# Optimization experiments

Hardware: AMD Instinct MI355X
Metric: run time of the kernel (lower is better)

Reference implementation:

```python
import jax, jax.numpy as jnp
import numpy as np

# Module constants derived from default grid_config
D = 59          # depth bins: (60-1)/1
C_OUT = 64
X, Y, Z = 128, 128, 7
STRIDE = 16
GRID_LB = np.array([-51.2, -51.2, -2.5], dtype=np.float32)
GRID_IV = np.array([0.8, 0.8, 1.0], dtype=np.float32)
D0, DSTEP = 1.0, 1.0

B, N, C_IN, H, W = 4, 6, 256, 16, 44


def _voxel_coords():
    xs, ys, zs = np.meshgrid(np.arange(X), np.arange(Y), np.arange(Z), indexing='ij')
    coords = np.stack([xs, ys, zs], axis=-1).reshape(-1, 3).astype(np.float32)
    coords = coords * GRID_IV + GRID_LB  # [V, 3] ego-frame voxel centers
    return coords


def _camera_rig(rng):
    """Realistic 6-camera rig: yawed cameras looking outward, z_cam = forward."""
    c2e = np.zeros((B, N, 4, 4), dtype=np.float32)
    K = np.zeros((B, N, 3, 3), dtype=np.float32)
    for b in range(B):
        for n in range(N):
            a = 2.0 * np.pi * n / N + 0.02 * rng.standard_normal()
            f = np.array([np.cos(a), np.sin(a), 0.0])           # camera forward (z_cam)
            x_cam = np.array([-np.sin(a), np.cos(a), 0.0])      # camera right
            y_cam = np.array([0.0, 0.0, -1.0])                   # camera down
            R = np.stack([x_cam, y_cam, f], axis=1)              # columns = cam axes in ego
            t = 1.0 * f + np.array([0.0, 0.0, 1.5])
            c2e[b, n, :3, :3] = R
            c2e[b, n, :3, 3] = t
            c2e[b, n, 3, 3] = 1.0
            fl = 400.0 + 5.0 * rng.standard_normal()
            K[b, n] = np.array([[fl, 0.0, 352.0], [0.0, fl, 128.0], [0.0, 0.0, 1.0]])
    return c2e, K


def setup_inputs() -> dict:
    key = jax.random.key(0)
    k1, k2, k3 = jax.random.split(key, 3)
    img_feats = jax.random.normal(k1, (B, N, C_IN, H, W), dtype=jnp.float32)
    c2e, K = _camera_rig(np.random.default_rng(0))
    # depth_net: 1x1 conv in_channels -> D + C_OUT
    w_depth = jax.random.normal(k2, (D + C_OUT, C_IN), dtype=jnp.float32) * (1.0 / np.sqrt(C_IN))
    b_depth = jax.random.normal(k3, (D + C_OUT,), dtype=jnp.float32) * 0.01
    return {
        'img_feats': img_feats,
        'cam2ego': jnp.asarray(c2e),
        'cam_intrinsics': jnp.asarray(K),
        'w_depth': w_depth,
        'b_depth': b_depth,
    }


def reference(img_feats, cam2ego, cam_intrinsics, w_depth, b_depth):
    Bc, Nc, C, Hc, Wc = img_feats.shape
    # 1x1 conv == per-pixel linear
    x = jnp.einsum('bnchw,oc->bnhwo', img_feats, w_depth) + b_depth  # [B,N,H,W,D+C_OUT]
    depth = jax.nn.softmax(x[..., :D], axis=-1)                      # [B,N,H,W,D]
    feat = x[..., D:]                                                # [B,N,H,W,C_OUT]

    vox = jnp.asarray(_voxel_coords())                               # [V,3]
    V = vox.shape[0]
    vox_h = jnp.concatenate([vox, jnp.ones((V, 1), vox.dtype)], axis=1)  # [V,4]

    e2c = jnp.linalg.inv(cam2ego)                                    # [B,N,4,4]
    cam = jnp.einsum('bnij,vj->bnvi', e2c, vox_h)[..., :3]           # [B,N,V,3]
    z = cam[..., 2]
    z_safe = jnp.maximum(z, 0.1)
    norm = cam[..., :2] / z_safe[..., None]
    homo = jnp.concatenate([norm, jnp.ones_like(z[..., None])], axis=-1)  # [B,N,V,3]
    img = jnp.einsum('bnij,bnvj->bnvi', cam_intrinsics, homo)[..., :2]
    fc = img / STRIDE                                                # feature-plane coords

    depth_bin = ((z - D0) / DSTEP).astype(jnp.int32)                 # trunc toward 0, matches .long()
    valid = (
        (fc[..., 0] >= 0) & (fc[..., 0] < Wc)
        & (fc[..., 1] >= 0) & (fc[..., 1] < Hc)
        & (z > 0.5)
        & (depth_bin >= 0) & (depth_bin < D)
    )

    u = jnp.clip(fc[..., 0].astype(jnp.int32), 0, Wc - 1)            # [B,N,V]
    v = jnp.clip(fc[..., 1].astype(jnp.int32), 0, Hc - 1)
    d = jnp.clip(depth_bin, 0, D - 1)
    hw = v * Wc + u

    feat_flat = feat.reshape(Bc, Nc, Hc * Wc, C_OUT)
    sampled_feat = jnp.take_along_axis(feat_flat, hw[..., None], axis=2)   # [B,N,V,C_OUT]
    depth_flat = depth.reshape(Bc, Nc, Hc * Wc * D)
    sampled_depth = jnp.take_along_axis(depth_flat, hw * D + d, axis=2)    # [B,N,V]

    wgt = sampled_depth * valid.astype(sampled_depth.dtype)
    # scatter_add at flat_idx == voxel index (identity) -> masked sum over cameras
    bev = jnp.einsum('bnv,bnvc->bvc', wgt, sampled_feat)             # [B,V,C_OUT]
    bev = bev.reshape(Bc, X, Y, Z, C_OUT).sum(axis=3)                # collapse Z
    bev = bev.transpose(0, 3, 2, 1)                                  # [B,C_OUT,Y,X]
    return bev, depth
```

## Files before the change

kernel.cpp:

```cpp
#include <hip/hip_runtime.h>
#include <math.h>

#define D_BINS 59
#define CO     64
#define CI     256
#define NB     4
#define NC     6
#define H_IMG  16
#define W_IMG  44
#define HW     704
#define NPIX   (NB*NC*HW)
#define XD     128
#define YD     128
#define ZD     7
#define NOUT   123
#define PXB    66
#define THR    384
#define XW     66

typedef float v2f __attribute__((ext_vector_type(2)));

__device__ void inv_rigid(const float* __restrict__ M, float* __restrict__ o) {
    double a = M[0], b = M[1], c = M[2], t0 = M[3];
    double d = M[4], e = M[5], f = M[6], t1 = M[7];
    double g = M[8], h = M[9], ii = M[10], t2 = M[11];
    double A00 = e*ii - f*h, A01 = c*h - b*ii, A02 = b*f - c*e;
    double A10 = f*g - d*ii, A11 = a*ii - c*g, A12 = c*d - a*f;
    double A20 = d*h - e*g,  A21 = b*g - a*h,  A22 = a*e - b*d;
    double det = a*A00 + b*A10 + c*A20;
    double inv = 1.0 / det;
    double r00 = A00*inv, r01 = A01*inv, r02 = A02*inv;
    double r10 = A10*inv, r11 = A11*inv, r12 = A12*inv;
    double r20 = A20*inv, r21 = A21*inv, r22 = A22*inv;
    o[0] = (float)r00; o[1] = (float)r01; o[2]  = (float)r02;
    o[3] = (float)(-(r00*t0 + r01*t1 + r02*t2));
    o[4] = (float)r10; o[5] = (float)r11; o[6]  = (float)r12;
    o[7] = (float)(-(r10*t0 + r11*t1 + r12*t2));
    o[8] = (float)r20; o[9] = (float)r21; o[10] = (float)r22;
    o[11] = (float)(-(r20*t0 + r21*t1 + r22*t2));
}

__global__ __launch_bounds__(256) void k_pre(
    const float* __restrict__ wd, const float* __restrict__ c2e,
    float* __restrict__ wt2, float* __restrict__ e2c) {
    const int o = blockIdx.x;
    const int k = threadIdx.x;
    float v = (o < NOUT) ? wd[(size_t)o * CI + k] : 0.f;
    wt2[(size_t)(k >> 1) * 256 + o * 2 + (k & 1)] = v;
    if (blockIdx.x == 0 && k < NB * NC)
        inv_rigid(c2e + k * 16, e2c + k * 12);
}

__global__ __launch_bounds__(THR) void k_head(
    const float* __restrict__ img, const float* __restrict__ wt2,
    const float* __restrict__ bd, float* __restrict__ depth_out,
    float* __restrict__ feat_ws) {
    __shared__ float A[64 / 2 * 132];
    __shared__ float X[PXB * XW];
    __shared__ float S[PXB];

    const int tid  = threadIdx.x;
    const int wv   = tid >> 6;
    const int ln   = tid & 63;
    const int p0   = blockIdx.x * PXB;
    const int half = blockIdx.y;
    const int ob   = half << 6;
    const bool is_main = (wv < 4);
    const int o0   = __builtin_amdgcn_readfirstlane(ob + ((is_main ? wv : 0) << 4));
    const int epx  = 64 + (wv - 4);

    int a_off[11];
    int g_off[11];
#pragma unroll
    for (int it = 0; it < 11; ++it) {
        int idx = tid + it * THR;
        int kl = idx / PXB, px = idx - kl * PXB;
        int p = p0 + px;
        int bn = p / HW, hw = p - bn * HW;
        a_off[it] = (kl >> 1) * 132 + px * 2 + (kl & 1);
        g_off[it] = (bn * CI + kl) * HW + hw;
    }

    v2f acc[16];
#pragma unroll
    for (int j = 0; j < 16; ++j) acc[j] = (v2f)(0.f);
    v2f acc2 = (v2f)(0.f);

    for (int kc = 0; kc < 4; ++kc) {
#pragma unroll
        for (int it = 0; it < 11; ++it)
            A[a_off[it]] = img[g_off[it] + kc * 64 * HW];
        __syncthreads();

        if (is_main) {
#pragma unroll 4
            for (int k2 = 0; k2 < 32; ++k2) {
                v2f a = *(const v2f*)(A + k2 * 132 + ln * 2);
                const v2f* w =
                    (const v2f*)(wt2 + (size_t)(kc * 32 + k2) * 256) + o0;
#pragma unroll
                for (int j = 0; j < 16; ++j)
                    acc[j] = __builtin_elementwise_fma(a, w[j], acc[j]);
            }
        } else {
#pragma unroll 4
            for (int k2 = 0; k2 < 32; ++k2) {
                v2f a = *(const v2f*)(A + k2 * 132 + epx * 2);
                const float* w = wt2 + (size_t)(kc * 32 + k2) * 256;
                v2f w0 = {w[(ob + ln) * 2], w[(ob + ln) * 2 + 1]};
                acc2 = __builtin_elementwise_fma(a, w0, acc2);
            }
        }
        __syncthreads();
    }

    if (is_main) {
#pragma unroll
        for (int j = 0; j < 16; ++j) {
            int o = o0 + j;
            if (o < NOUT)
                X[ln * XW + (o - ob)] = (acc[j].x + acc[j].y) + bd[o];
        }
    } else {
        int o = ob + ln;
        if (o < NOUT)
            X[epx * XW + ln] = (acc2.x + acc2.y) + bd[o];
    }
    __syncthreads();

    if (half == 0) {
        if (tid < PXB * 5) {
            int p = tid / 5, c = tid - p * 5;
            feat_ws[(size_t)(p0 + p) * CO + c] = X[p * XW + 59 + c];
        }
        if (tid < PXB) {
            float* row = X + tid * XW;
            float m = row[0];
            for (int o = 1; o < D_BINS; ++o) m = fmaxf(m, row[o]);
            float s = 0.f;
            for (int o = 0; o < D_BINS; ++o) {
                float e = __expf(row[o] - m);
                row[o] = e;
                s += e;
            }
            S[tid] = 1.f / s;
        }
        __syncthreads();
        for (int g = tid; g < PXB * D_BINS; g += THR) {
            int p = g / D_BINS;
            int o = g - p * D_BINS;
            depth_out[(size_t)p0 * D_BINS + g] = X[p * XW + o] * S[p];
        }
    } else {
        for (int g = tid; g < PXB * D_BINS; g += THR) {
            int p = g / D_BINS;
            int col = g - p * D_BINS;
            feat_ws[(size_t)(p0 + p) * CO + 5 + col] = X[p * XW + col];
        }
    }
}

__global__ __launch_bounds__(256) void k_splat(
    const float* __restrict__ e2c, const float* __restrict__ Kmat,
    const float* __restrict__ depth_g, const float* __restrict__ feat_ws,
    float* __restrict__ bev) {
    __shared__ int   hw_s[ZD][64];
    __shared__ float wgt_s[ZD][64];

    const int tx = threadIdx.x;
    const int cq = threadIdx.y;
    const int x = blockIdx.x * 64 + tx;
    const int y = blockIdx.y;
    const int b = blockIdx.z;
    const float wx = (float)x * 0.8f + (-51.2f);
    const float wy = (float)y * 0.8f + (-51.2f);

    float acc[16];
#pragma unroll
    for (int m = 0; m < 16; ++m) acc[m] = 0.f;

    for (int n = 0; n < NC; ++n) {
        const int bn = b * NC + n;
        const float* E = e2c + bn * 12;
        const float* Km = Kmat + bn * 9;
        const float k00 = Km[0], k01 = Km[1], k02 = Km[2];
        const float k10 = Km[3], k11 = Km[4], k12 = Km[5];
        const float e02 = E[2], e12 = E[6], e22 = E[10];
        const float bx0 = E[0] * wx + E[1] * wy + E[3];
        const float bx1 = E[4] * wx + E[5] * wy + E[7];
        const float bx2 = E[8] * wx + E[9] * wy + E[11];

#pragma unroll
        for (int zz = 0; zz < 2; ++zz) {
            const int z = cq + zz * 4;
            if (z < ZD) {
                const float wz = -2.5f + (float)z;
                const float cx = bx0 + e02 * wz;
                const float cy = bx1 + e12 * wz;
                const float cz = bx2 + e22 * wz;
                const float zs = fmaxf(cz, 0.1f);
                const float rz = 1.0f / zs;
                const float xn = cx * rz;
                const float yn = cy * rz;
                const float fu = (k00 * xn + k01 * yn + k02) * 0.0625f;
                const float fv = (k10 * xn + k11 * yn + k12) * 0.0625f;
                const int bin = (int)(cz - 1.0f);
                const bool valid = (fu >= 0.f) & (fu < (float)W_IMG) &
                                   (fv >= 0.f) & (fv < (float)H_IMG) &
                                   (cz > 0.5f) & (bin >= 0) & (bin < D_BINS);
                int hw = -1;
                float wgt = 0.f;
                if (valid) {
                    int u = (int)fu;
                    int v = (int)fv;
                    hw = v * W_IMG + u;
                    wgt = depth_g[((size_t)bn * HW + hw) * D_BINS + bin];
                }
                hw_s[z][tx] = hw;
                wgt_s[z][tx] = wgt;
            }
        }
        __syncthreads();

#pragma unroll
        for (int z = 0; z < ZD; ++z) {
            const int hw = hw_s[z][tx];
            if (hw >= 0) {
                const float wgt = wgt_s[z][tx];
                const float4* fp =
                    (const float4*)(feat_ws + ((size_t)bn * HW + hw) * CO + cq * 16);
                float4 f0 = fp[0], f1 = fp[1], f2 = fp[2], f3 = fp[3];
                acc[0]  = fmaf(wgt, f0.x, acc[0]);
                acc[1]  = fmaf(wgt, f0.y, acc[1]);
                acc[2]  = fmaf(wgt, f0.z, acc[2]);
                acc[3]  = fmaf(wgt, f0.w, acc[3]);
                acc[4]  = fmaf(wgt, f1.x, acc[4]);
                acc[5]  = fmaf(wgt, f1.y, acc[5]);
                acc[6]  = fmaf(wgt, f1.z, acc[6]);
                acc[7]  = fmaf(wgt, f1.w, acc[7]);
                acc[8]  = fmaf(wgt, f2.x, acc[8]);
                acc[9]  = fmaf(wgt, f2.y, acc[9]);
                acc[10] = fmaf(wgt, f2.z, acc[10]);
                acc[11] = fmaf(wgt, f2.w, acc[11]);
                acc[12] = fmaf(wgt, f3.x, acc[12]);
                acc[13] = fmaf(wgt, f3.y, acc[13]);
                acc[14] = fmaf(wgt, f3.z, acc[14]);
                acc[15] = fmaf(wgt, f3.w, acc[15]);
            }
        }
        __syncthreads();
    }
    float* ob = bev + (((size_t)b * CO + cq * 16) * YD + y) * XD + x;
#pragma unroll
    for (int m = 0; m < 16; ++m) ob[(size_t)m * YD * XD] = acc[m];
}

extern "C" void kernel_launch(void* const* d_in, const int* in_sizes, int n_in,
                              void* d_out, int out_size, void* d_ws, size_t ws_size,
                              hipStream_t stream) {
    const float* img  = (const float*)d_in[0];
    const float* c2e  = (const float*)d_in[1];
    const float* Kmat = (const float*)d_in[2];
    const float* wd   = (const float*)d_in[3];
    const float* bd   = (const float*)d_in[4];
    float* bev = (float*)d_out;
    float* depth_out = bev + (size_t)NB * CO * YD * XD;
    float* feat_ws = (float*)d_ws;
    float* wt2 = feat_ws + (size_t)NPIX * CO;
    float* e2c = wt2 + 128 * 256;

    k_pre<<<128, 256, 0, stream>>>(wd, c2e, wt2, e2c);
    k_head<<<dim3(256, 2), THR, 0, stream>>>(img, wt2, bd, depth_out, feat_ws);
    k_splat<<<dim3(2, YD, NB), dim3(64, 4, 1), 0, stream>>>(e2c, Kmat, depth_out,
                                                            feat_ws, bev);
}
```

Measured before the change: 122.5 us.

## Split K across two wave groups and load full input tile once

```diff
diff --git a/kernel.cpp b/kernel.cpp
--- a/kernel.cpp
+++ b/kernel.cpp
@@ -15,7 +15,7 @@
 #define ZD     7
 #define NOUT   123
 #define PXB    66
-#define THR    384
+#define THR    768
 #define XW     66
 
 typedef float v2f __attribute__((ext_vector_type(2)));
@@ -55,9 +55,8 @@
     const float* __restrict__ img, const float* __restrict__ wt2,
     const float* __restrict__ bd, float* __restrict__ depth_out,
     float* __restrict__ feat_ws) {
-    __shared__ float A[64 / 2 * 132];
-    __shared__ float X[PXB * XW];
-    __shared__ float S[PXB];
+    __shared__ float smem[128 * 132 + PXB];
+    float* S = smem + 128 * 132;
 
     const int tid  = threadIdx.x;
     const int wv   = tid >> 6;
@@ -65,66 +64,82 @@
     const int p0   = blockIdx.x * PXB;
     const int half = blockIdx.y;
     const int ob   = half << 6;
-    const bool is_main = (wv < 4);
-    const int o0   = __builtin_amdgcn_readfirstlane(ob + ((is_main ? wv : 0) << 4));
-    const int epx  = 64 + (wv - 4);
-
-    int a_off[11];
-    int g_off[11];
-#pragma unroll
-    for (int it = 0; it < 11; ++it) {
-        int idx = tid + it * THR;
+    const bool is_main = (wv < 8);
+    const int j    = wv & 3;
+    const int kh   = is_main ? (wv >> 2) : ((wv - 8) >> 1);
+    const int o0   = __builtin_amdgcn_readfirstlane(ob + (j << 4));
+    const int k2b  = __builtin_amdgcn_readfirstlane(kh << 6);
+    const int epx  = __builtin_amdgcn_readfirstlane(64 + ((wv - 8) & 1));
+
+    for (int idx = tid; idx < 256 * PXB; idx += THR) {
         int kl = idx / PXB, px = idx - kl * PXB;
         int p = p0 + px;
         int bn = p / HW, hw = p - bn * HW;
-        a_off[it] = (kl >> 1) * 132 + px * 2 + (kl & 1);
-        g_off[it] = (bn * CI + kl) * HW + hw;
-    }
+        smem[(kl >> 1) * 132 + px * 2 + (kl & 1)] =
+            img[((size_t)bn * CI + kl) * HW + hw];
+    }
+    __syncthreads();
 
     v2f acc[16];
 #pragma unroll
-    for (int j = 0; j < 16; ++j) acc[j] = (v2f)(0.f);
+    for (int q = 0; q < 16; ++q) acc[q] = (v2f)(0.f);
     v2f acc2 = (v2f)(0.f);
 
-    for (int kc = 0; kc < 4; ++kc) {
-#pragma unroll
-        for (int it = 0; it < 11; ++it)
-            A[a_off[it]] = img[g_off[it] + kc * 64 * HW];
-        __syncthreads();
-
+    if (is_main) {
+#pragma unroll 4
+        for (int k2i = 0; k2i < 64; ++k2i) {
+            int k2 = k2b + k2i;
+            v2f a = *(const v2f*)(smem + k2 * 132 + ln * 2);
+            const v2f* w = (const v2f*)(wt2 + (size_t)k2 * 256) + o0;
+#pragma unroll
+            for (int q = 0; q < 16; ++q)
+                acc[q] = __builtin_elementwise_fma(a, w[q], acc[q]);
+        }
+    } else {
+#pragma unroll 4
+        for (int k2i = 0; k2i < 64; ++k2i) {
+            int k2 = k2b + k2i;
+            v2f a = *(const v2f*)(smem + k2 * 132 + epx * 2);
+            const float* w = wt2 + (size_t)k2 * 256;
+            v2f w0 = {w[(ob + ln) * 2], w[(ob + ln) * 2 + 1]};
+            acc2 = __builtin_elementwise_fma(a, w0, acc2);
+        }
+    }
+    __syncthreads();
+
+    float* X = smem;
+    if (kh == 0) {
         if (is_main) {
-#pragma unroll 4
-            for (int k2 = 0; k2 < 32; ++k2) {
-                v2f a = *(const v2f*)(A + k2 * 132 + ln * 2);
-                const v2f* w =
-                    (const v2f*)(wt2 + (size_t)(kc * 32 + k2) * 256) + o0;
-#pragma unroll
-                for (int j = 0; j < 16; ++j)
-                    acc[j] = __builtin_elementwise_fma(a, w[j], acc[j]);
+#pragma unroll
+            for (int q = 0; q < 16; ++q) {
+                int o = o0 + q;
+                if (o < NOUT)
+                    X[ln * XW + (o - ob)] = acc[q].x + acc[q].y;
             }
         } else {
-#pragma unroll 4
-            for (int k2 = 0; k2 < 32; ++k2) {
-                v2f a = *(const v2f*)(A + k2 * 132 + epx * 2);
-                const float* w = wt2 + (size_t)(kc * 32 + k2) * 256;
-                v2f w0 = {w[(ob + ln) * 2], w[(ob + ln) * 2 + 1]};
-                acc2 = __builtin_elementwise_fma(a, w0, acc2);
-            }
-        }
-        __syncthreads();
-    }
-
-    if (is_main) {
-#pragma unroll
-        for (int j = 0; j < 16; ++j) {
-            int o = o0 + j;
+            int o = ob + ln;
             if (o < NOUT)
-                X[ln * XW + (o - ob)] = (acc[j].x + acc[j].y) + bd[o];
-        }
-    } else {
-        int o = ob + ln;
-        if (o < NOUT)
-            X[epx * XW + ln] = (acc2.x + acc2.y) + bd[o];
+                X[epx * XW + ln] = acc2.x + acc2.y;
+        }
+    }
+    __syncthreads();
+    if (kh == 1) {
+        if (is_main) {
+#pragma unroll
+            for (int q = 0; q < 16; ++q) {
+                int o = o0 + q;
+                if (o < NOUT) {
+                    int col = o - ob;
+                    X[ln * XW + col] =
+                        (X[ln * XW + col] + (acc[q].x + acc[q].y)) + bd[o];
+                }
+            }
+        } else {
+            int o = ob + ln;
+            if (o < NOUT)
+                X[epx * XW + ln] =
+                    (X[epx * XW + ln] + (acc2.x + acc2.y)) + bd[o];
+        }
     }
     __syncthreads();
 
```

Result: slower. 131.4 us (+7.2%).

## Double pixels per head block to reuse weight loads across two pixel sets

Applied to the files above, without the earlier changes.

```diff
diff --git a/kernel.cpp b/kernel.cpp
--- a/kernel.cpp
+++ b/kernel.cpp
@@ -14,7 +14,7 @@
 #define YD     128
 #define ZD     7
 #define NOUT   123
-#define PXB    66
+#define PXB    132
 #define THR    384
 #define XW     66
 
@@ -55,82 +55,89 @@
     const float* __restrict__ img, const float* __restrict__ wt2,
     const float* __restrict__ bd, float* __restrict__ depth_out,
     float* __restrict__ feat_ws) {
-    __shared__ float A[64 / 2 * 132];
-    __shared__ float X[PXB * XW];
-    __shared__ float S[PXB];
+    __shared__ float smem[PXB * XW + PXB];
+    float* S = smem + PXB * XW;
 
     const int tid  = threadIdx.x;
     const int wv   = tid >> 6;
     const int ln   = tid & 63;
     const int p0   = blockIdx.x * PXB;
-    const int half = blockIdx.y;
-    const int ob   = half << 6;
+    const int ob   = (int)blockIdx.y << 6;
     const bool is_main = (wv < 4);
     const int o0   = __builtin_amdgcn_readfirstlane(ob + ((is_main ? wv : 0) << 4));
-    const int epx  = 64 + (wv - 4);
-
-    int a_off[11];
-    int g_off[11];
-#pragma unroll
-    for (int it = 0; it < 11; ++it) {
-        int idx = tid + it * THR;
-        int kl = idx / PXB, px = idx - kl * PXB;
-        int p = p0 + px;
-        int bn = p / HW, hw = p - bn * HW;
-        a_off[it] = (kl >> 1) * 132 + px * 2 + (kl & 1);
-        g_off[it] = (bn * CI + kl) * HW + hw;
-    }
-
-    v2f acc[16];
-#pragma unroll
-    for (int j = 0; j < 16; ++j) acc[j] = (v2f)(0.f);
-    v2f acc2 = (v2f)(0.f);
-
+    const int e0   = 128 + (wv - 4);
+    const int e1   = 130 + (wv - 4);
+
+    v2f accA[16], accB[16];
+#pragma unroll
+    for (int j = 0; j < 16; ++j) { accA[j] = (v2f)(0.f); accB[j] = (v2f)(0.f); }
+    v2f acc2a = (v2f)(0.f), acc2b = (v2f)(0.f);
+
+    float* A = smem;
     for (int kc = 0; kc < 4; ++kc) {
 #pragma unroll
-        for (int it = 0; it < 11; ++it)
-            A[a_off[it]] = img[g_off[it] + kc * 64 * HW];
+        for (int it = 0; it < 22; ++it) {
+            int idx = tid + it * THR;
+            int kl = idx / PXB, px = idx - kl * PXB;
+            int p = p0 + px;
+            int bn = p / HW, hw = p - bn * HW;
+            A[(kl >> 1) * 264 + px * 2 + (kl & 1)] =
+                img[((size_t)bn * CI + kc * 64 + kl) * HW + hw];
+        }
         __syncthreads();
 
         if (is_main) {
 #pragma unroll 4
             for (int k2 = 0; k2 < 32; ++k2) {
-                v2f a = *(const v2f*)(A + k2 * 132 + ln * 2);
+                v2f aA = *(const v2f*)(A + k2 * 264 + ln * 2);
+                v2f aB = *(const v2f*)(A + k2 * 264 + (ln + 64) * 2);
                 const v2f* w =
                     (const v2f*)(wt2 + (size_t)(kc * 32 + k2) * 256) + o0;
 #pragma unroll
-                for (int j = 0; j < 16; ++j)
-                    acc[j] = __builtin_elementwise_fma(a, w[j], acc[j]);
+                for (int j = 0; j < 16; ++j) {
+                    v2f wj = w[j];
+                    accA[j] = __builtin_elementwise_fma(aA, wj, accA[j]);
+                    accB[j] = __builtin_elementwise_fma(aB, wj, accB[j]);
+                }
             }
         } else {
 #pragma unroll 4
             for (int k2 = 0; k2 < 32; ++k2) {
-                v2f a = *(const v2f*)(A + k2 * 132 + epx * 2);
+                v2f a0 = *(const v2f*)(A + k2 * 264 + e0 * 2);
+                v2f a1 = *(const v2f*)(A + k2 * 264 + e1 * 2);
                 const float* w = wt2 + (size_t)(kc * 32 + k2) * 256;
                 v2f w0 = {w[(ob + ln) * 2], w[(ob + ln) * 2 + 1]};
-                acc2 = __builtin_elementwise_fma(a, w0, acc2);
-            }
-        }
-        __syncthreads();
-    }
-
+                acc2a = __builtin_elementwise_fma(a0, w0, acc2a);
+                acc2b = __builtin_elementwise_fma(a1, w0, acc2b);
+            }
+        }
+        __syncthreads();
+    }
+
+    float* X = smem;
     if (is_main) {
 #pragma unroll
         for (int j = 0; j < 16; ++j) {
             int o = o0 + j;
-            if (o < NOUT)
-                X[ln * XW + (o - ob)] = (acc[j].x + acc[j].y) + bd[o];
+            if (o < NOUT) {
+                int col = o - ob;
+                X[ln * XW + col]        = (accA[j].x + accA[j].y) + bd[o];
+                X[(ln + 64) * XW + col] = (accB[j].x + accB[j].y) + bd[o];
+            }
         }
     } else {
         int o = ob + ln;
-        if (o < NOUT)
-            X[epx * XW + ln] = (acc2.x + acc2.y) + bd[o];
+        if (o < NOUT) {
+            int col = o - ob;
+            X[e0 * XW + col] = (acc2a.x + acc2a.y) + bd[o];
+            X[e1 * XW + col] = (acc2b.x + acc2b.y) + bd[o];
+        }
     }
     __syncthreads();
 
-    if (half == 0) {
-        if (tid < PXB * 5) {
-            int p = tid / 5, c = tid - p * 5;
+    if (blockIdx.y == 0) {
+        for (int g = tid; g < PXB * 5; g += THR) {
+            int p = g / 5, c = g - p * 5;
             feat_ws[(size_t)(p0 + p) * CO + c] = X[p * XW + 59 + c];
         }
         if (tid < PXB) {
@@ -270,7 +277,7 @@
     float* e2c = wt2 + 128 * 256;
 
     k_pre<<<128, 256, 0, stream>>>(wd, c2e, wt2, e2c);
-    k_head<<<dim3(256, 2), THR, 0, stream>>>(img, wt2, bd, depth_out, feat_ws);
+    k_head<<<dim3(128, 2), THR, 0, stream>>>(img, wt2, bd, depth_out, feat_ws);
     k_splat<<<dim3(2, YD, NB), dim3(64, 4, 1), 0, stream>>>(e2c, Kmat, depth_out,
                                                             feat_ws, bev);
 }
```

Result: slower. 133.5 us (+9.0%).
